# Kernel tuning notes

Measured on AMD Instinct MI355X. Metric: run time of the kernel, lower is better.

## Reference

```python
import jax, jax.numpy as jnp
import numpy as np

L, H, N = 131072, 256, 128
P = N // 2  # conj-symmetric half state


def _hippo_params(p_sz, h_sz):
    # create_DPLR_HiPPO(block_size) in numpy (float64 eigh, then cast)
    n = np.arange(p_sz)
    pv = np.sqrt(1.0 + 2.0 * n)
    A = -(np.tril(np.outer(pv, pv)) - np.diag(n))          # make_HiPPO
    Pl = np.sqrt(n + 0.5)
    Bl = np.sqrt(2.0 * n + 1.0)
    S = A + np.outer(Pl, Pl)                                # normal part
    lam_re = np.full(p_sz, S.diagonal().mean())
    lam_im, V = np.linalg.eigh(S * (-1j))
    Lambda = lam_re + 1j * lam_im                           # (P,)
    Vinv = V.conj().T
    rng = np.random.default_rng(0)
    B0 = rng.normal(size=(p_sz, h_sz)) / np.sqrt(h_sz)      # lecun-normal-ish
    Bc = Vinv @ B0                                          # init_VinvB -> (P,H) complex
    C0 = rng.normal(size=(h_sz, p_sz)) / np.sqrt(p_sz)
    Cc = C0 @ V                                             # init_CV -> (H,P) complex
    Dv = rng.normal(size=(h_sz,))
    return Lambda, Bc, Cc, Dv


def setup_inputs() -> dict:
    Lambda, Bc, Cc, Dv = _hippo_params(P, H)
    deltas = np.logspace(-3.0, -1.0, P)
    key = jax.random.key(0)
    ku, kd = jax.random.split(key)
    u = jax.random.normal(ku, (L, H), dtype=jnp.float32)
    d = jax.random.bernoulli(kd, 1.0 / 1024.0, (L,))        # sparse episode resets
    f32 = lambda a: jnp.asarray(a, dtype=jnp.float32)
    return {
        "u": u,
        "Lambda_re": f32(Lambda.real), "Lambda_im": f32(Lambda.imag),
        "B_re": f32(Bc.real), "B_im": f32(Bc.imag),
        "C_re": f32(Cc.real), "C_im": f32(Cc.imag),
        "D": f32(Dv),
        "deltas": f32(deltas),
        "x0_re": jnp.zeros((P,), jnp.float32), "x0_im": jnp.zeros((P,), jnp.float32),
        "d": d,
    }


def reference(u, Lambda_re, Lambda_im, B_re, B_im, C_re, C_im, D, deltas,
              x0_re, x0_im, d):
    cplx = jnp.complex64
    Lambda = (Lambda_re + 1j * Lambda_im).astype(cplx)      # (P,)
    B = (B_re + 1j * B_im).astype(cplx)                     # (P,H)
    C = (C_re + 1j * C_im).astype(cplx)                     # (H,P)
    x0 = (x0_re + 1j * x0_im).astype(cplx)                  # (P,)

    # ZOH discretization
    Lambda_bar = jnp.exp(Lambda * deltas)                   # (P,)
    B_bar = ((Lambda_bar - 1.0) / Lambda)[:, None] * B      # (P,H)

    Bu = u.astype(cplx) @ B_bar.T                           # (L,P)

    Lseq = u.shape[0]
    A_el = jnp.concatenate([jnp.ones((1, Lambda_bar.shape[0]), cplx),
                            jnp.broadcast_to(Lambda_bar, (Lseq, Lambda_bar.shape[0]))])
    b_el = jnp.concatenate([x0[None, :], Bu])
    d_el = jnp.concatenate([jnp.zeros((1,), bool), d])

    def comb(qi, qj):
        Ai, bi, di = qi
        Aj, bj, dj = qj
        m = dj[..., None]
        A = jnp.where(m, Aj, Aj * Ai)
        b = jnp.where(m, bj, Aj * bi + bj)
        return (A, b, jnp.logical_or(di, dj))

    _, xs, _ = jax.lax.associative_scan(comb, (A_el, b_el, d_el))
    xs = xs[1:]                                             # (L,P)

    # conj-symmetric readout: y = 2*Re(C x) + D*u
    y = 2.0 * (xs @ C.T).real + u * D                       # (L,H)
    return y
```

## Files before the change

### kernel.cpp

```cpp
#include <hip/hip_runtime.h>
#include <hip/hip_bf16.h>
#include <stdint.h>

#define L_SEQ 131072
#define H_DIM 256
#define P_DIM 64
#define C2    128
#define T_CH  128
#define NC    1024
#define SUBT  32
#define BPAD  136

typedef unsigned short u16t;
typedef __attribute__((ext_vector_type(8))) short short8;
typedef __attribute__((ext_vector_type(4))) float f32x4;

#define OFF_W2_U   32768u
#define OFF_LPRE_F 32768u
#define OFF_LPIM_F 40960u
#define OFF_LAMB_F 49152u
#define OFF_FR_I   49408u
#define OFF_CL_F   50432u
#define OFF_XIN_F  181504u
#define OFF_U16_B  2097152u

__device__ __forceinline__ float bf2f(unsigned v){
    return __builtin_bit_cast(float, v << 16);
}
__device__ __forceinline__ u16t f2bf16(float f){
    uint32_t u = __builtin_bit_cast(uint32_t, f);
    u += 0x7fffu + ((u >> 16) & 1u);
    return (u16t)(u >> 16);
}
__device__ __forceinline__ unsigned pk2(float a, float b){
    return (unsigned)f2bf16(a) | ((unsigned)f2bf16(b) << 16);
}

__global__ __launch_bounds__(256) void kconv(const float* __restrict__ u,
                                             u16t* __restrict__ o){
    const size_t n = (size_t)L_SEQ * H_DIM / 8;
    size_t i = (size_t)blockIdx.x * 256 + threadIdx.x;
    const size_t step = (size_t)gridDim.x * 256;
    for (; i < n; i += step){
        const float* p = u + i*8;
        float4 a = *(const float4*)p;
        float4 b = *(const float4*)(p + 4);
        uint4 o4;
        o4.x = pk2(a.x, a.y); o4.y = pk2(a.z, a.w);
        o4.z = pk2(b.x, b.y); o4.w = pk2(b.z, b.w);
        *(uint4*)(o + i*8) = o4;
    }
}

__global__ void k0a(const float* __restrict__ Lre, const float* __restrict__ Lim,
                    const float* __restrict__ deltas, float* __restrict__ wsf){
    int p = threadIdx.x;
    if (p >= P_DIM) return;
    float lr = Lre[p], li = Lim[p], dl = deltas[p];
    float er = expf(lr * dl);
    float si, co;
    sincosf(li * dl, &si, &co);
    float lbr = er * co, lbi = er * si;
    float den = lr*lr + li*li;
    float gr = ((lbr - 1.f)*lr + lbi*li) / den;
    float gi = (lbi*lr - (lbr - 1.f)*li) / den;
    float* lamb = wsf + OFF_LAMB_F;
    lamb[p] = lbr; lamb[64+p] = lbi; lamb[128+p] = gr; lamb[192+p] = gi;
    float* lpre = wsf + OFF_LPRE_F;
    float* lpim = wsf + OFF_LPIM_F;
    float pr = lbr, pi = lbi;
    for (int k = 0; k < T_CH; k++){
        lpre[k*64 + p] = pr;
        lpim[k*64 + p] = pi;
        float nr = pr*lbr - pi*lbi;
        float ni = pr*lbi + pi*lbr;
        pr = nr; pi = ni;
    }
}

__global__ void k0b(const float* __restrict__ Bre, const float* __restrict__ Bim,
                    const float* __restrict__ Cre, const float* __restrict__ Cim,
                    float* __restrict__ wsf, u16t* __restrict__ wsu){
    int idx = blockIdx.x * 256 + threadIdx.x;
    const float* lamb = wsf + OFF_LAMB_F;
    if (idx < 32768){
        int c = idx >> 8, h = idx & 255;
        int p = c & 63;
        float gr = lamb[128+p], gi = lamb[192+p];
        float br = Bre[p*H_DIM + h], bi = Bim[p*H_DIM + h];
        float v = (c < 64) ? (gr*br - gi*bi) : (gr*bi + gi*br);
        wsu[idx] = f2bf16(v);
    } else {
        int i2 = idx - 32768;
        int h = i2 >> 7, c = i2 & 127;
        float v = (c < 64) ? 2.f * Cre[h*P_DIM + c] : -2.f * Cim[h*P_DIM + (c-64)];
        wsu[OFF_W2_U + i2] = f2bf16(v);
    }
}

template<bool USE_U16>
__global__ __launch_bounds__(256, 3) void k1(const float* __restrict__ u,
                                             const u16t* __restrict__ u16g,
                                             const int* __restrict__ dflag,
                                             float* __restrict__ wsf,
                                             u16t* __restrict__ wsu){
    __shared__ u16t  buf[T_CH * BPAD];
    __shared__ int   d_lds[T_CH];
    __shared__ float sublast[4*128];
    __shared__ int   sfr[4];

    const int tid  = threadIdx.x;
    const int w    = tid >> 6, lane = tid & 63;
    const int m    = lane & 15, q = lane >> 4;
    const int cc   = blockIdx.x;
    const int t0   = cc * T_CH;
    const int tg   = t0 + w * SUBT;

    if (tid < T_CH) d_lds[tid] = dflag[t0 + tid];

    uint4 ap[16];
    #pragma unroll
    for (int kf = 0; kf < 8; kf++){
        #pragma unroll
        for (int mt = 0; mt < 2; mt++){
            if (USE_U16){
                ap[kf*2+mt] = *(const uint4*)(u16g + (size_t)(tg + mt*16 + m)*H_DIM + kf*32 + q*8);
            } else {
                const float* apn = u + (size_t)(tg + mt*16 + m)*H_DIM + kf*32 + q*8;
                float4 f0 = *(const float4*)apn;
                float4 f1 = *(const float4*)(apn + 4);
                uint4 pk;
                pk.x = pk2(f0.x, f0.y); pk.y = pk2(f0.z, f0.w);
                pk.z = pk2(f1.x, f1.y); pk.w = pk2(f1.z, f1.w);
                ap[kf*2+mt] = pk;
            }
        }
    }

    const u16t* W1 = wsu;
    f32x4 acc[2][8];
    #pragma unroll
    for (int a = 0; a < 2; a++)
        #pragma unroll
        for (int b = 0; b < 8; b++) acc[a][b] = (f32x4){0.f,0.f,0.f,0.f};

    #pragma unroll
    for (int kf = 0; kf < 8; kf++){
        const int k0 = kf*32 + q*8;
        short8 a0 = __builtin_bit_cast(short8, ap[kf*2+0]);
        short8 a1 = __builtin_bit_cast(short8, ap[kf*2+1]);
        #pragma unroll
        for (int nt = 0; nt < 8; nt++){
            short8 bfr = __builtin_bit_cast(short8, *(const uint4*)(W1 + (nt*16 + m)*H_DIM + k0));
            acc[0][nt] = __builtin_amdgcn_mfma_f32_16x16x32_bf16(a0, bfr, acc[0][nt], 0,0,0);
            acc[1][nt] = __builtin_amdgcn_mfma_f32_16x16x32_bf16(a1, bfr, acc[1][nt], 0,0,0);
        }
    }
    #pragma unroll
    for (int mt = 0; mt < 2; mt++)
        #pragma unroll
        for (int nt = 0; nt < 8; nt++){
            int c  = nt*16 + m;
            int tl = w*SUBT + mt*16 + q*4;
            #pragma unroll
            for (int r = 0; r < 4; r++)
                buf[(tl + r)*BPAD + c] = f2bf16(acc[mt][nt][r]);
        }
    __syncthreads();

    {
        const float* lamb = wsf + OFF_LAMB_F;
        float lbr = lamb[lane], lbi = lamb[64 + lane];
        float xr = 0.f, xi = 0.f;
        int frs = SUBT;
        const int base = w * SUBT;
        for (int tt = 0; tt < SUBT; tt++){
            int tl = base + tt;
            float br = bf2f(buf[tl*BPAD + lane]);
            float bi = bf2f(buf[tl*BPAD + 64 + lane]);
            if (d_lds[tl]){
                if (frs == SUBT) frs = tt;
                xr = br; xi = bi;
            } else {
                float nr = fmaf(lbr, xr, fmaf(-lbi, xi, br));
                float ni = fmaf(lbr, xi, fmaf( lbi, xr, bi));
                xr = nr; xi = ni;
            }
        }
        sublast[w*128 + lane]      = xr;
        sublast[w*128 + 64 + lane] = xi;
        if (lane == 0) sfr[w] = frs;
    }
    __syncthreads();

    if (tid < 64){
        const float* lpre = wsf + OFF_LPRE_F;
        const float* lpim = wsf + OFF_LPIM_F;
        float l32r = lpre[(SUBT-1)*64 + tid], l32i = lpim[(SUBT-1)*64 + tid];
        float xr = 0.f, xi = 0.f;
        int fr_c = T_CH;
        #pragma unroll
        for (int w2 = 0; w2 < 4; w2++){
            float sr = sublast[w2*128 + tid], si = sublast[w2*128 + 64 + tid];
            int f = sfr[w2];
            if (f < SUBT){
                xr = sr; xi = si;
                if (fr_c == T_CH) fr_c = w2*SUBT + f;
            } else {
                float nr = fmaf(l32r, xr, fmaf(-l32i, xi, sr));
                float ni = fmaf(l32r, xi, fmaf( l32i, xr, si));
                xr = nr; xi = ni;
            }
        }
        float* clast = wsf + OFF_CL_F;
        clast[cc*128 + tid]      = xr;
        clast[cc*128 + 64 + tid] = xi;
        if (tid == 0) ((int*)wsf)[OFF_FR_I + cc] = fr_c;
    }
}

__global__ void k2(const float* __restrict__ x0re, const float* __restrict__ x0im,
                   float* __restrict__ wsf){
    const int p = threadIdx.x;
    const float* clast = wsf + OFF_CL_F;
    const int*   frg   = (const int*)wsf + OFF_FR_I;
    float*       xin   = wsf + OFF_XIN_F;
    const float ltr = (wsf + OFF_LPRE_F)[127*64 + p];
    const float lti = (wsf + OFF_LPIM_F)[127*64 + p];
    float xr = x0re[p], xi = x0im[p];
    const int G = 16;
    float br[G], bi[G], br2[G], bi2[G]; int fr[G], fr2[G];

    auto ldg = [&](int cb, float* A, float* B, int* F){
        #pragma unroll
        for (int j = 0; j < G; j++){
            A[j] = clast[(cb+j)*128 + p];
            B[j] = clast[(cb+j)*128 + 64 + p];
            F[j] = frg[cb+j];
        }
    };
    ldg(0, br, bi, fr);
    for (int g = 0; g < NC / G; g++){
        int cb = g * G;
        if (g + 1 < NC / G) ldg(cb + G, br2, bi2, fr2);
        #pragma unroll
        for (int j = 0; j < G; j++){
            xin[(cb+j)*128 + p]      = xr;
            xin[(cb+j)*128 + 64 + p] = xi;
            if (fr[j] < T_CH){ xr = br[j]; xi = bi[j]; }
            else {
                float nr = fmaf(ltr, xr, fmaf(-lti, xi, br[j]));
                float ni = fmaf(ltr, xi, fmaf( lti, xr, bi[j]));
                xr = nr; xi = ni;
            }
        }
        #pragma unroll
        for (int j = 0; j < G; j++){ br[j]=br2[j]; bi[j]=bi2[j]; fr[j]=fr2[j]; }
    }
}

template<bool USE_U16>
__global__ __launch_bounds__(256, 2) void k3(const float* __restrict__ u,
                                             const u16t* __restrict__ u16g,
                                             const int* __restrict__ dflag,
                                             const float* __restrict__ D,
                                             float* __restrict__ wsf,
                                             u16t* __restrict__ wsu,
                                             float* __restrict__ y){
    __shared__ u16t  buf[T_CH * BPAD];
    __shared__ int   d_lds[T_CH];
    __shared__ float sublast[4*128];
    __shared__ float xin_s[4*128];
    __shared__ int   sfr[4];

    const int tid  = threadIdx.x;
    const int w    = tid >> 6, lane = tid & 63;
    const int m    = lane & 15, q = lane >> 4;
    const int cc   = blockIdx.x;
    const int t0   = cc * T_CH;
    const int tg   = t0 + w * SUBT;

    if (tid < T_CH) d_lds[tid] = dflag[t0 + tid];

    {
        uint4 ap[16];
        #pragma unroll
        for (int kf = 0; kf < 8; kf++){
            #pragma unroll
            for (int mt = 0; mt < 2; mt++){
                if (USE_U16){
                    ap[kf*2+mt] = *(const uint4*)(u16g + (size_t)(tg + mt*16 + m)*H_DIM + kf*32 + q*8);
                } else {
                    const float* apn = u + (size_t)(tg + mt*16 + m)*H_DIM + kf*32 + q*8;
                    float4 f0 = *(const float4*)apn;
                    float4 f1 = *(const float4*)(apn + 4);
                    uint4 pk;
                    pk.x = pk2(f0.x, f0.y); pk.y = pk2(f0.z, f0.w);
                    pk.z = pk2(f1.x, f1.y); pk.w = pk2(f1.z, f1.w);
                    ap[kf*2+mt] = pk;
                }
            }
        }
        const u16t* W1 = wsu;
        f32x4 acc[2][8];
        #pragma unroll
        for (int a = 0; a < 2; a++)
            #pragma unroll
            for (int b = 0; b < 8; b++) acc[a][b] = (f32x4){0.f,0.f,0.f,0.f};

        #pragma unroll
        for (int kf = 0; kf < 8; kf++){
            const int k0 = kf*32 + q*8;
            short8 a0 = __builtin_bit_cast(short8, ap[kf*2+0]);
            short8 a1 = __builtin_bit_cast(short8, ap[kf*2+1]);
            #pragma unroll
            for (int nt = 0; nt < 8; nt++){
                short8 bfr = __builtin_bit_cast(short8, *(const uint4*)(W1 + (nt*16 + m)*H_DIM + k0));
                acc[0][nt] = __builtin_amdgcn_mfma_f32_16x16x32_bf16(a0, bfr, acc[0][nt], 0,0,0);
                acc[1][nt] = __builtin_amdgcn_mfma_f32_16x16x32_bf16(a1, bfr, acc[1][nt], 0,0,0);
            }
        }
        #pragma unroll
        for (int mt = 0; mt < 2; mt++)
            #pragma unroll
            for (int nt = 0; nt < 8; nt++){
                int c  = nt*16 + m;
                int tl = w*SUBT + mt*16 + q*4;
                #pragma unroll
                for (int r = 0; r < 4; r++)
                    buf[(tl + r)*BPAD + c] = f2bf16(acc[mt][nt][r]);
            }
    }
    __syncthreads();

    {
        const float* lamb = wsf + OFF_LAMB_F;
        float lbr = lamb[lane], lbi = lamb[64 + lane];
        float xr = 0.f, xi = 0.f;
        int frs = SUBT;
        const int base = w * SUBT;
        for (int tt = 0; tt < SUBT; tt++){
            int tl = base + tt;
            float br = bf2f(buf[tl*BPAD + lane]);
            float bi = bf2f(buf[tl*BPAD + 64 + lane]);
            if (d_lds[tl]){
                if (frs == SUBT) frs = tt;
                xr = br; xi = bi;
            } else {
                float nr = fmaf(lbr, xr, fmaf(-lbi, xi, br));
                float ni = fmaf(lbr, xi, fmaf( lbi, xr, bi));
                xr = nr; xi = ni;
            }
            buf[tl*BPAD + lane]      = f2bf16(xr);
            buf[tl*BPAD + 64 + lane] = f2bf16(xi);
        }
        sublast[w*128 + lane]      = xr;
        sublast[w*128 + 64 + lane] = xi;
        if (lane == 0) sfr[w] = frs;
    }
    __syncthreads();

    if (tid < 64){
        const float* lpre = wsf + OFF_LPRE_F;
        const float* lpim = wsf + OFF_LPIM_F;
        const float* xin  = wsf + OFF_XIN_F;
        float l32r = lpre[(SUBT-1)*64 + tid], l32i = lpim[(SUBT-1)*64 + tid];
        float xr = xin[cc*128 + tid], xi = xin[cc*128 + 64 + tid];
        #pragma unroll
        for (int w2 = 0; w2 < 4; w2++){
            xin_s[w2*128 + tid]      = xr;
            xin_s[w2*128 + 64 + tid] = xi;
            float sr = sublast[w2*128 + tid], si = sublast[w2*128 + 64 + tid];
            if (sfr[w2] < SUBT){ xr = sr; xi = si; }
            else {
                float nr = fmaf(l32r, xr, fmaf(-l32i, xi, sr));
                float ni = fmaf(l32r, xi, fmaf( l32i, xr, si));
                xr = nr; xi = ni;
            }
        }
    }
    __syncthreads();

    {
        const float* lpre = wsf + OFF_LPRE_F;
        const float* lpim = wsf + OFF_LPIM_F;
        #pragma unroll 4
        for (int i = 0; i < 32; i++){
            int idx = i*256 + tid;
            int tl = idx >> 6, j = idx & 63;
            int c0 = j*2;
            int w2 = tl >> 5, tt = tl & 31;
            if (tt < sfr[w2]){
                unsigned pr = *(unsigned*)&buf[tl*BPAD + c0];
                float v0 = bf2f(pr & 0xffffu), v1 = bf2f(pr >> 16);
                int p0 = c0 & 63;
                float lr0 = lpre[tt*64 + p0], lr1 = lpre[tt*64 + p0 + 1];
                float li0 = lpim[tt*64 + p0], li1 = lpim[tt*64 + p0 + 1];
                float xr0 = xin_s[w2*128 + p0],      xr1 = xin_s[w2*128 + p0 + 1];
                float xi0 = xin_s[w2*128 + 64 + p0], xi1 = xin_s[w2*128 + 64 + p0 + 1];
                if (c0 < 64){
                    v0 += lr0*xr0 - li0*xi0;
                    v1 += lr1*xr1 - li1*xi1;
                } else {
                    v0 += lr0*xi0 + li0*xr0;
                    v1 += lr1*xi1 + li1*xr1;
                }
                *(unsigned*)&buf[tl*BPAD + c0] = pk2(v0, v1);
            }
        }
    }
    __syncthreads();

    f32x4 acc2[2][16];
    #pragma unroll
    for (int a = 0; a < 2; a++)
        #pragma unroll
        for (int b = 0; b < 16; b++) acc2[a][b] = (f32x4){0.f,0.f,0.f,0.f};
    {
        const u16t* W2 = wsu + OFF_W2_U;
        #pragma unroll
        for (int ng = 0; ng < 4; ng++){
            #pragma unroll
            for (int kf = 0; kf < 4; kf++){
                const int k0 = kf*32 + q*8;
                short8 a0 = *(const short8*)&buf[(w*SUBT +  0 + m)*BPAD + k0];
                short8 a1 = *(const short8*)&buf[(w*SUBT + 16 + m)*BPAD + k0];
                #pragma unroll
                for (int nj = 0; nj < 4; nj++){
                    int nt = ng*4 + nj;
                    short8 bfr = __builtin_bit_cast(short8, *(const uint4*)(W2 + (nt*16 + m)*C2 + k0));
                    acc2[0][nt] = __builtin_amdgcn_mfma_f32_16x16x32_bf16(a0, bfr, acc2[0][nt], 0,0,0);
                    acc2[1][nt] = __builtin_amdgcn_mfma_f32_16x16x32_bf16(a1, bfr, acc2[1][nt], 0,0,0);
                }
            }
        }
    }

    #pragma unroll
    for (int nt = 0; nt < 16; nt++){
        int h = nt*16 + m;
        float dv = D[h];
        #pragma unroll
        for (int mt = 0; mt < 2; mt++){
            int tb = tg + mt*16 + q*4;
            #pragma unroll
            for (int r = 0; r < 4; r++){
                float uv = USE_U16 ? bf2f(u16g[(size_t)(tb + r)*H_DIM + h])
                                   : u[(size_t)(tb + r)*H_DIM + h];
                y[(size_t)(tb + r)*H_DIM + h] = fmaf(uv, dv, acc2[mt][nt][r]);
            }
        }
    }
}

extern "C" void kernel_launch(void* const* d_in, const int* in_sizes, int n_in,
                              void* d_out, int out_size, void* d_ws, size_t ws_size,
                              hipStream_t stream){
    const float* u      = (const float*)d_in[0];
    const float* Lre    = (const float*)d_in[1];
    const float* Lim    = (const float*)d_in[2];
    const float* Bre    = (const float*)d_in[3];
    const float* Bim    = (const float*)d_in[4];
    const float* Cre    = (const float*)d_in[5];
    const float* Cim    = (const float*)d_in[6];
    const float* D      = (const float*)d_in[7];
    const float* x0re   = (const float*)d_in[9];
    const float* x0im   = (const float*)d_in[10];
    const int*   dflag  = (const int*)d_in[11];
    const float* deltas = (const float*)d_in[8];
    float* wsf = (float*)d_ws;
    u16t*  wsu = (u16t*)d_ws;
    u16t*  u16g = (u16t*)((char*)d_ws + OFF_U16_B);
    float* y   = (float*)d_out;

    const size_t need = (size_t)OFF_U16_B + (size_t)L_SEQ * H_DIM * 2;
    const bool use16 = (ws_size >= need);

    k0a<<<1, 64, 0, stream>>>(Lre, Lim, deltas, wsf);
    k0b<<<256, 256, 0, stream>>>(Bre, Bim, Cre, Cim, wsf, wsu);
    if (use16){
        kconv<<<4096, 256, 0, stream>>>(u, u16g);
        k1<true ><<<NC, 256, 0, stream>>>(u, u16g, dflag, wsf, wsu);
        k2<<<1, 64, 0, stream>>>(x0re, x0im, wsf);
        k3<true ><<<NC, 256, 0, stream>>>(u, u16g, dflag, D, wsf, wsu, y);
    } else {
        k1<false><<<NC, 256, 0, stream>>>(u, u16g, dflag, wsf, wsu);
        k2<<<1, 64, 0, stream>>>(x0re, x0im, wsf);
        k3<false><<<NC, 256, 0, stream>>>(u, u16g, dflag, D, wsf, wsu, y);
    }
}
```

Before: 452.0 us.

## Store chunk-local scan states in k1 and drop recompute in k3

Result: faster. 408.5 us (-9.6%).

```diff
diff --git a/kernel.cpp b/kernel.cpp
--- a/kernel.cpp
+++ b/kernel.cpp
@@ -22,7 +22,9 @@
 #define OFF_FR_I   49408u
 #define OFF_CL_F   50432u
 #define OFF_XIN_F  181504u
-#define OFF_U16_B  2097152u
+#define OFF_SL_F   312576u
+#define OFF_SFR_I  836864u
+#define OFF_XL_U   1681920u
 
 __device__ __forceinline__ float bf2f(unsigned v){
     return __builtin_bit_cast(float, v << 16);
@@ -36,77 +38,61 @@
     return (unsigned)f2bf16(a) | ((unsigned)f2bf16(b) << 16);
 }
 
-__global__ __launch_bounds__(256) void kconv(const float* __restrict__ u,
-                                             u16t* __restrict__ o){
-    const size_t n = (size_t)L_SEQ * H_DIM / 8;
-    size_t i = (size_t)blockIdx.x * 256 + threadIdx.x;
-    const size_t step = (size_t)gridDim.x * 256;
-    for (; i < n; i += step){
-        const float* p = u + i*8;
-        float4 a = *(const float4*)p;
-        float4 b = *(const float4*)(p + 4);
-        uint4 o4;
-        o4.x = pk2(a.x, a.y); o4.y = pk2(a.z, a.w);
-        o4.z = pk2(b.x, b.y); o4.w = pk2(b.z, b.w);
-        *(uint4*)(o + i*8) = o4;
-    }
-}
-
-__global__ void k0a(const float* __restrict__ Lre, const float* __restrict__ Lim,
-                    const float* __restrict__ deltas, float* __restrict__ wsf){
-    int p = threadIdx.x;
-    if (p >= P_DIM) return;
-    float lr = Lre[p], li = Lim[p], dl = deltas[p];
-    float er = expf(lr * dl);
-    float si, co;
-    sincosf(li * dl, &si, &co);
-    float lbr = er * co, lbi = er * si;
-    float den = lr*lr + li*li;
-    float gr = ((lbr - 1.f)*lr + lbi*li) / den;
-    float gi = (lbi*lr - (lbr - 1.f)*li) / den;
-    float* lamb = wsf + OFF_LAMB_F;
-    lamb[p] = lbr; lamb[64+p] = lbi; lamb[128+p] = gr; lamb[192+p] = gi;
-    float* lpre = wsf + OFF_LPRE_F;
-    float* lpim = wsf + OFF_LPIM_F;
-    float pr = lbr, pi = lbi;
-    for (int k = 0; k < T_CH; k++){
-        lpre[k*64 + p] = pr;
-        lpim[k*64 + p] = pi;
-        float nr = pr*lbr - pi*lbi;
-        float ni = pr*lbi + pi*lbr;
-        pr = nr; pi = ni;
-    }
-}
-
-__global__ void k0b(const float* __restrict__ Bre, const float* __restrict__ Bim,
-                    const float* __restrict__ Cre, const float* __restrict__ Cim,
-                    float* __restrict__ wsf, u16t* __restrict__ wsu){
-    int idx = blockIdx.x * 256 + threadIdx.x;
-    const float* lamb = wsf + OFF_LAMB_F;
-    if (idx < 32768){
-        int c = idx >> 8, h = idx & 255;
-        int p = c & 63;
-        float gr = lamb[128+p], gi = lamb[192+p];
+__global__ void k0(const float* __restrict__ Lre, const float* __restrict__ Lim,
+                   const float* __restrict__ deltas,
+                   const float* __restrict__ Bre, const float* __restrict__ Bim,
+                   const float* __restrict__ Cre, const float* __restrict__ Cim,
+                   float* __restrict__ wsf, u16t* __restrict__ wsu){
+    const int b = blockIdx.x, tid = threadIdx.x;
+    if (b == 0 && tid < P_DIM){
+        const int p = tid;
+        float lr = Lre[p], li = Lim[p], dl = deltas[p];
+        float er = expf(lr * dl);
+        float si, co; sincosf(li * dl, &si, &co);
+        float lbr = er * co, lbi = er * si;
+        float den = lr*lr + li*li;
+        float gr = ((lbr - 1.f)*lr + lbi*li) / den;
+        float gi = (lbi*lr - (lbr - 1.f)*li) / den;
+        float* lamb = wsf + OFF_LAMB_F;
+        lamb[p] = lbr; lamb[64+p] = lbi; lamb[128+p] = gr; lamb[192+p] = gi;
+        float* lpre = wsf + OFF_LPRE_F;
+        float* lpim = wsf + OFF_LPIM_F;
+        float pr = lbr, pi = lbi;
+        for (int k = 0; k < T_CH; k++){
+            lpre[k*64 + p] = pr;
+            lpim[k*64 + p] = pi;
+            float nr = pr*lbr - pi*lbi;
+            float ni = pr*lbi + pi*lbr;
+            pr = nr; pi = ni;
+        }
+    }
+    if (b < 128){
+        const int c = b, h = tid, p = c & 63;
+        float lr = Lre[p], li = Lim[p], dl = deltas[p];
+        float er = expf(lr * dl);
+        float si, co; sincosf(li * dl, &si, &co);
+        float lbr = er * co, lbi = er * si;
+        float den = lr*lr + li*li;
+        float gr = ((lbr - 1.f)*lr + lbi*li) / den;
+        float gi = (lbi*lr - (lbr - 1.f)*li) / den;
         float br = Bre[p*H_DIM + h], bi = Bim[p*H_DIM + h];
         float v = (c < 64) ? (gr*br - gi*bi) : (gr*bi + gi*br);
-        wsu[idx] = f2bf16(v);
+        wsu[c*H_DIM + h] = f2bf16(v);
     } else {
-        int i2 = idx - 32768;
+        int i2 = (b - 128)*256 + tid;
         int h = i2 >> 7, c = i2 & 127;
         float v = (c < 64) ? 2.f * Cre[h*P_DIM + c] : -2.f * Cim[h*P_DIM + (c-64)];
         wsu[OFF_W2_U + i2] = f2bf16(v);
     }
 }
 
-template<bool USE_U16>
 __global__ __launch_bounds__(256, 3) void k1(const float* __restrict__ u,
-                                             const u16t* __restrict__ u16g,
                                              const int* __restrict__ dflag,
                                              float* __restrict__ wsf,
                                              u16t* __restrict__ wsu){
-    __shared__ u16t  buf[T_CH * BPAD];
+    __shared__ __align__(16) u16t buf[T_CH * BPAD];
     __shared__ int   d_lds[T_CH];
-    __shared__ float sublast[4*128];
+    __shared__ __align__(16) float sublast[4*128];
     __shared__ int   sfr[4];
 
     const int tid  = threadIdx.x;
@@ -123,17 +109,13 @@
     for (int kf = 0; kf < 8; kf++){
         #pragma unroll
         for (int mt = 0; mt < 2; mt++){
-            if (USE_U16){
-                ap[kf*2+mt] = *(const uint4*)(u16g + (size_t)(tg + mt*16 + m)*H_DIM + kf*32 + q*8);
-            } else {
-                const float* apn = u + (size_t)(tg + mt*16 + m)*H_DIM + kf*32 + q*8;
-                float4 f0 = *(const float4*)apn;
-                float4 f1 = *(const float4*)(apn + 4);
-                uint4 pk;
-                pk.x = pk2(f0.x, f0.y); pk.y = pk2(f0.z, f0.w);
-                pk.z = pk2(f1.x, f1.y); pk.w = pk2(f1.z, f1.w);
-                ap[kf*2+mt] = pk;
-            }
+            const float* apn = u + (size_t)(tg + mt*16 + m)*H_DIM + kf*32 + q*8;
+            float4 f0 = *(const float4*)apn;
+            float4 f1 = *(const float4*)(apn + 4);
+            uint4 pk;
+            pk.x = pk2(f0.x, f0.y); pk.y = pk2(f0.z, f0.w);
+            pk.z = pk2(f1.x, f1.y); pk.w = pk2(f1.z, f1.w);
+            ap[kf*2+mt] = pk;
         }
     }
 
@@ -142,16 +124,16 @@
     #pragma unroll
     for (int a = 0; a < 2; a++)
         #pragma unroll
-        for (int b = 0; b < 8; b++) acc[a][b] = (f32x4){0.f,0.f,0.f,0.f};
+        for (int bb = 0; bb < 8; bb++) acc[a][bb] = (f32x4){0.f,0.f,0.f,0.f};
 
     #pragma unroll
     for (int kf = 0; kf < 8; kf++){
-        const int k0 = kf*32 + q*8;
+        const int k0v = kf*32 + q*8;
         short8 a0 = __builtin_bit_cast(short8, ap[kf*2+0]);
         short8 a1 = __builtin_bit_cast(short8, ap[kf*2+1]);
         #pragma unroll
         for (int nt = 0; nt < 8; nt++){
-            short8 bfr = __builtin_bit_cast(short8, *(const uint4*)(W1 + (nt*16 + m)*H_DIM + k0));
+            short8 bfr = __builtin_bit_cast(short8, *(const uint4*)(W1 + (nt*16 + m)*H_DIM + k0v));
             acc[0][nt] = __builtin_amdgcn_mfma_f32_16x16x32_bf16(a0, bfr, acc[0][nt], 0,0,0);
             acc[1][nt] = __builtin_amdgcn_mfma_f32_16x16x32_bf16(a1, bfr, acc[1][nt], 0,0,0);
         }
@@ -186,12 +168,28 @@
                 float ni = fmaf(lbr, xi, fmaf( lbi, xr, bi));
                 xr = nr; xi = ni;
             }
+            buf[tl*BPAD + lane]      = f2bf16(xr);
+            buf[tl*BPAD + 64 + lane] = f2bf16(xi);
         }
         sublast[w*128 + lane]      = xr;
         sublast[w*128 + 64 + lane] = xi;
         if (lane == 0) sfr[w] = frs;
     }
     __syncthreads();
+
+    {
+        u16t* xl = wsu + OFF_XL_U + (size_t)t0 * C2;
+        #pragma unroll
+        for (int i = 0; i < 8; i++){
+            int idx = i*256 + tid;
+            int row = idx >> 4, c16 = idx & 15;
+            *(uint4*)(xl + row*C2 + c16*8) = *(const uint4*)&buf[row*BPAD + c16*8];
+        }
+    }
+    if (tid < 128)
+        *(float4*)(wsf + OFF_SL_F + (size_t)cc*512 + tid*4) = *(const float4*)&sublast[tid*4];
+    if (tid < 4)
+        ((int*)wsf)[OFF_SFR_I + cc*4 + tid] = sfr[tid];
 
     if (tid < 64){
         const float* lpre = wsf + OFF_LPRE_F;
@@ -259,19 +257,14 @@
     }
 }
 
-template<bool USE_U16>
 __global__ __launch_bounds__(256, 2) void k3(const float* __restrict__ u,
-                                             const u16t* __restrict__ u16g,
-                                             const int* __restrict__ dflag,
                                              const float* __restrict__ D,
                                              float* __restrict__ wsf,
                                              u16t* __restrict__ wsu,
                                              float* __restrict__ y){
-    __shared__ u16t  buf[T_CH * BPAD];
-    __shared__ int   d_lds[T_CH];
-    __shared__ float sublast[4*128];
+    __shared__ __align__(16) u16t buf[T_CH * BPAD];
     __shared__ float xin_s[4*128];
-    __shared__ int   sfr[4];
+    __shared__ int   sfr_s[4];
 
     const int tid  = threadIdx.x;
     const int w    = tid >> 6, lane = tid & 63;
@@ -280,98 +273,36 @@
     const int t0   = cc * T_CH;
     const int tg   = t0 + w * SUBT;
 
-    if (tid < T_CH) d_lds[tid] = dflag[t0 + tid];
-
-    {
-        uint4 ap[16];
-        #pragma unroll
-        for (int kf = 0; kf < 8; kf++){
-            #pragma unroll
-            for (int mt = 0; mt < 2; mt++){
-                if (USE_U16){
-                    ap[kf*2+mt] = *(const uint4*)(u16g + (size_t)(tg + mt*16 + m)*H_DIM + kf*32 + q*8);
-                } else {
-                    const float* apn = u + (size_t)(tg + mt*16 + m)*H_DIM + kf*32 + q*8;
-                    float4 f0 = *(const float4*)apn;
-                    float4 f1 = *(const float4*)(apn + 4);
-                    uint4 pk;
-                    pk.x = pk2(f0.x, f0.y); pk.y = pk2(f0.z, f0.w);
-                    pk.z = pk2(f1.x, f1.y); pk.w = pk2(f1.z, f1.w);
-                    ap[kf*2+mt] = pk;
-                }
-            }
-        }
-        const u16t* W1 = wsu;
-        f32x4 acc[2][8];
-        #pragma unroll
-        for (int a = 0; a < 2; a++)
-            #pragma unroll
-            for (int b = 0; b < 8; b++) acc[a][b] = (f32x4){0.f,0.f,0.f,0.f};
-
-        #pragma unroll
-        for (int kf = 0; kf < 8; kf++){
-            const int k0 = kf*32 + q*8;
-            short8 a0 = __builtin_bit_cast(short8, ap[kf*2+0]);
-            short8 a1 = __builtin_bit_cast(short8, ap[kf*2+1]);
-            #pragma unroll
-            for (int nt = 0; nt < 8; nt++){
-                short8 bfr = __builtin_bit_cast(short8, *(const uint4*)(W1 + (nt*16 + m)*H_DIM + k0));
-                acc[0][nt] = __builtin_amdgcn_mfma_f32_16x16x32_bf16(a0, bfr, acc[0][nt], 0,0,0);
-                acc[1][nt] = __builtin_amdgcn_mfma_f32_16x16x32_bf16(a1, bfr, acc[1][nt], 0,0,0);
-            }
-        }
-        #pragma unroll
-        for (int mt = 0; mt < 2; mt++)
-            #pragma unroll
-            for (int nt = 0; nt < 8; nt++){
-                int c  = nt*16 + m;
-                int tl = w*SUBT + mt*16 + q*4;
-                #pragma unroll
-                for (int r = 0; r < 4; r++)
-                    buf[(tl + r)*BPAD + c] = f2bf16(acc[mt][nt][r]);
-            }
-    }
-    __syncthreads();
-
-    {
-        const float* lamb = wsf + OFF_LAMB_F;
-        float lbr = lamb[lane], lbi = lamb[64 + lane];
-        float xr = 0.f, xi = 0.f;
-        int frs = SUBT;
-        const int base = w * SUBT;
-        for (int tt = 0; tt < SUBT; tt++){
-            int tl = base + tt;
-            float br = bf2f(buf[tl*BPAD + lane]);
-            float bi = bf2f(buf[tl*BPAD + 64 + lane]);
-            if (d_lds[tl]){
-                if (frs == SUBT) frs = tt;
-                xr = br; xi = bi;
-            } else {
-                float nr = fmaf(lbr, xr, fmaf(-lbi, xi, br));
-                float ni = fmaf(lbr, xi, fmaf( lbi, xr, bi));
-                xr = nr; xi = ni;
-            }
-            buf[tl*BPAD + lane]      = f2bf16(xr);
-            buf[tl*BPAD + 64 + lane] = f2bf16(xi);
-        }
-        sublast[w*128 + lane]      = xr;
-        sublast[w*128 + 64 + lane] = xi;
-        if (lane == 0) sfr[w] = frs;
-    }
-    __syncthreads();
+    {
+        const u16t* xl = wsu + OFF_XL_U + (size_t)t0 * C2;
+        uint4 st[8];
+        #pragma unroll
+        for (int i = 0; i < 8; i++){
+            int idx = i*256 + tid;
+            st[i] = *(const uint4*)(xl + (idx >> 4)*C2 + (idx & 15)*8);
+        }
+        #pragma unroll
+        for (int i = 0; i < 8; i++){
+            int idx = i*256 + tid;
+            *(uint4*)&buf[(idx >> 4)*BPAD + (idx & 15)*8] = st[i];
+        }
+    }
+    if (tid < 4) sfr_s[tid] = ((const int*)wsf)[OFF_SFR_I + cc*4 + tid];
 
     if (tid < 64){
         const float* lpre = wsf + OFF_LPRE_F;
         const float* lpim = wsf + OFF_LPIM_F;
         const float* xin  = wsf + OFF_XIN_F;
+        const float* gsl  = wsf + OFF_SL_F + (size_t)cc*512;
+        const int*   gsfr = (const int*)wsf + OFF_SFR_I + cc*4;
         float l32r = lpre[(SUBT-1)*64 + tid], l32i = lpim[(SUBT-1)*64 + tid];
         float xr = xin[cc*128 + tid], xi = xin[cc*128 + 64 + tid];
         #pragma unroll
         for (int w2 = 0; w2 < 4; w2++){
             xin_s[w2*128 + tid]      = xr;
             xin_s[w2*128 + 64 + tid] = xi;
-            float sr = sublast[w2*128 + tid], si = sublast[w2*128 + 64 + tid];
-            if (sfr[w2] < SUBT){ xr = sr; xi = si; }
+            float sr = gsl[w2*128 + tid], si = gsl[w2*128 + 64 + tid];
+            if (gsfr[w2] < SUBT){ xr = sr; xi = si; }
             else {
                 float nr = fmaf(l32r, xr, fmaf(-l32i, xi, sr));
                 float ni = fmaf(l32r, xi, fmaf( l32i, xr, si));
@@ -390,7 +321,7 @@
             int tl = idx >> 6, j = idx & 63;
             int c0 = j*2;
             int w2 = tl >> 5, tt = tl & 31;
-            if (tt < sfr[w2]){
+            if (tt < sfr_s[w2]){
                 unsigned pr = *(unsigned*)&buf[tl*BPAD + c0];
                 float v0 = bf2f(pr & 0xffffu), v1 = bf2f(pr >> 16);
                 int p0 = c0 & 63;
@@ -415,39 +346,66 @@
     #pragma unroll
     for (int a = 0; a < 2; a++)
         #pragma unroll
-        for (int b = 0; b < 16; b++) acc2[a][b] = (f32x4){0.f,0.f,0.f,0.f};
+        for (int bb = 0; bb < 16; bb++) acc2[a][bb] = (f32x4){0.f,0.f,0.f,0.f};
     {
         const u16t* W2 = wsu + OFF_W2_U;
         #pragma unroll
         for (int ng = 0; ng < 4; ng++){
             #pragma unroll
             for (int kf = 0; kf < 4; kf++){
-                const int k0 = kf*32 + q*8;
-                short8 a0 = *(const short8*)&buf[(w*SUBT +  0 + m)*BPAD + k0];
-                short8 a1 = *(const short8*)&buf[(w*SUBT + 16 + m)*BPAD + k0];
+                const int k0v = kf*32 + q*8;
+                short8 a0 = *(const short8*)&buf[(w*SUBT +  0 + m)*BPAD + k0v];
+                short8 a1 = *(const short8*)&buf[(w*SUBT + 16 + m)*BPAD + k0v];
                 #pragma unroll
                 for (int nj = 0; nj < 4; nj++){
                     int nt = ng*4 + nj;
-                    short8 bfr = __builtin_bit_cast(short8, *(const uint4*)(W2 + (nt*16 + m)*C2 + k0));
+                    short8 bfr = __builtin_bit_cast(short8, *(const uint4*)(W2 + (nt*16 + m)*C2 + k0v));
                     acc2[0][nt] = __builtin_amdgcn_mfma_f32_16x16x32_bf16(a0, bfr, acc2[0][nt], 0,0,0);
                     acc2[1][nt] = __builtin_amdgcn_mfma_f32_16x16x32_bf16(a1, bfr, acc2[1][nt], 0,0,0);
                 }
             }
         }
     }
-
-    #pragma unroll
-    for (int nt = 0; nt < 16; nt++){
-        int h = nt*16 + m;
-        float dv = D[h];
+    __syncthreads();
+
+    {
+        float* ep = (float*)&buf[w * SUBT * BPAD];
+        float4 dv4[4];
+        #pragma unroll
+        for (int hj = 0; hj < 4; hj++)
+            dv4[hj] = *(const float4*)(D + (hj >> 1)*128 + (hj & 1)*64 + m*4);
+
         #pragma unroll
         for (int mt = 0; mt < 2; mt++){
-            int tb = tg + mt*16 + q*4;
             #pragma unroll
-            for (int r = 0; r < 4; r++){
-                float uv = USE_U16 ? bf2f(u16g[(size_t)(tb + r)*H_DIM + h])
-                                   : u[(size_t)(tb + r)*H_DIM + h];
-                y[(size_t)(tb + r)*H_DIM + h] = fmaf(uv, dv, acc2[mt][nt][r]);
+            for (int half = 0; half < 2; half++){
+                #pragma unroll
+                for (int n2 = 0; n2 < 8; n2++){
+                    int nt = half*8 + n2;
+                    #pragma unroll
+                    for (int r = 0; r < 4; r++)
+                        ep[(q*4 + r)*132 + n2*16 + m] = acc2[mt][nt][r];
+                }
+                __syncthreads();
+                #pragma unroll
+                for (int i = 0; i < 4; i++){
+                    int row = q + i*4;
+                    size_t t = (size_t)(tg + mt*16 + row);
+                    #pragma unroll
+                    for (int j = 0; j < 2; j++){
+                        int col = j*64 + m*4;
+                        float4 v  = *(const float4*)&ep[row*132 + col];
+                        float4 uu = *(const float4*)(u + t*H_DIM + half*128 + col);
+                        float4 dd = dv4[half*2 + j];
+                        float4 o;
+                        o.x = fmaf(uu.x, dd.x, v.x);
+                        o.y = fmaf(uu.y, dd.y, v.y);
+                        o.z = fmaf(uu.z, dd.z, v.z);
+                        o.w = fmaf(uu.w, dd.w, v.w);
+                        *(float4*)(y + t*H_DIM + half*128 + col) = o;
+                    }
+                }
+                __syncthreads();
             }
         }
     }
@@ -456,6 +414,7 @@
 extern "C" void kernel_launch(void* const* d_in, const int* in_sizes, int n_in,
                               void* d_out, int out_size, void* d_ws, size_t ws_size,
                               hipStream_t stream){
+    (void)in_sizes; (void)n_in; (void)out_size; (void)ws_size;
     const float* u      = (const float*)d_in[0];
     const float* Lre    = (const float*)d_in[1];
     const float* Lim    = (const float*)d_in[2];
@@ -464,28 +423,16 @@
     const float* Cre    = (const float*)d_in[5];
     const float* Cim    = (const float*)d_in[6];
     const float* D      = (const float*)d_in[7];
+    const float* deltas = (const float*)d_in[8];
     const float* x0re   = (const float*)d_in[9];
     const float* x0im   = (const float*)d_in[10];
     const int*   dflag  = (const int*)d_in[11];
-    const float* deltas = (const float*)d_in[8];
     float* wsf = (float*)d_ws;
     u16t*  wsu = (u16t*)d_ws;
-    u16t*  u16g = (u16t*)((char*)d_ws + OFF_U16_B);
     float* y   = (float*)d_out;
 
-    const size_t need = (size_t)OFF_U16_B + (size_t)L_SEQ * H_DIM * 2;
-    const bool use16 = (ws_size >= need);
-
-    k0a<<<1, 64, 0, stream>>>(Lre, Lim, deltas, wsf);
-    k0b<<<256, 256, 0, stream>>>(Bre, Bim, Cre, Cim, wsf, wsu);
-    if (use16){
-        kconv<<<4096, 256, 0, stream>>>(u, u16g);
-        k1<true ><<<NC, 256, 0, stream>>>(u, u16g, dflag, wsf, wsu);
-        k2<<<1, 64, 0, stream>>>(x0re, x0im, wsf);
-        k3<true ><<<NC, 256, 0, stream>>>(u, u16g, dflag, D, wsf, wsu, y);
-    } else {
-        k1<false><<<NC, 256, 0, stream>>>(u, u16g, dflag, wsf, wsu);
-        k2<<<1, 64, 0, stream>>>(x0re, x0im, wsf);
-        k3<false><<<NC, 256, 0, stream>>>(u, u16g, dflag, D, wsf, wsu, y);
-    }
-}
+    k0<<<256, 256, 0, stream>>>(Lre, Lim, deltas, Bre, Bim, Cre, Cim, wsf, wsu);
+    k1<<<NC, 256, 0, stream>>>(u, dflag, wsf, wsu);
+    k2<<<1, 64, 0, stream>>>(x0re, x0im, wsf);
+    k3<<<NC, 256, 0, stream>>>(u, D, wsf, wsu, y);
+}
```
